# Performance work log

Measured on AMD Instinct MI355X. Metric: run time of the kernel, lower is better.

The kernel has to match this reference:

```python
import jax, jax.numpy as jnp
import numpy as np

L, B, S, M, D, H, DK, FF = 4, 2, 512, 512, 1024, 16, 64, 4096


def setup_inputs() -> dict:
    key = jax.random.key(0)
    ks = jax.random.split(key, 16)
    std = 0.02
    inp = {
        'x': jax.random.normal(ks[0], (B, S, D), jnp.float32),
        'memory': jax.random.normal(ks[1], (L, B, M, D), jnp.float32),
        'Wq': jax.random.normal(ks[2], (L, D, D), jnp.float32) * std,
        'Wk': jax.random.normal(ks[3], (L, D, D), jnp.float32) * std,
        'Wv': jax.random.normal(ks[4], (L, D, D), jnp.float32) * std,
        'Wr': jax.random.normal(ks[5], (L, D, D), jnp.float32) * std,
        'Wo': jax.random.normal(ks[6], (L, D, D), jnp.float32) * std,
        'r_w_bias': jax.random.normal(ks[7], (L, H, DK), jnp.float32) * std,
        'r_r_bias': jax.random.normal(ks[8], (L, H, DK), jnp.float32) * std,
        'ln1_g': jnp.ones((L, D), jnp.float32),
        'ln1_b': jnp.zeros((L, D), jnp.float32),
        'ln2_g': jnp.ones((L, D), jnp.float32),
        'ln2_b': jnp.zeros((L, D), jnp.float32),
        'W1': jax.random.normal(ks[9], (L, D, FF), jnp.float32) * std,
        'b1': jnp.zeros((L, FF), jnp.float32),
        'W2': jax.random.normal(ks[10], (L, FF, D), jnp.float32) * std,
        'b2': jnp.zeros((L, D), jnp.float32),
    }
    return inp


def _pos_encodings(length, hidden):
    # sinusoidal encodings over [length-1 .. 0], sin/cos concat -> [length, hidden]
    pos = jnp.arange(length - 1, -1, -1, dtype=jnp.float32)
    freqs = jnp.arange(0, hidden, 2, dtype=jnp.float32)
    inv_freq = 1.0 / (10000.0 ** (freqs / hidden))
    ang = pos[:, None] * inv_freq[None, :]  # [T, D/2]
    return jnp.concatenate([jnp.sin(ang), jnp.cos(ang)], axis=-1)  # [T, D]


def _rel_shift(x):
    # x: [B, H, T1, T2] -> Transformer-XL relative shift
    b, h, t1, t2 = x.shape
    x = jnp.pad(x, ((0, 0), (0, 0), (0, 0), (1, 0)))
    x = x.reshape(b, h, t2 + 1, t1)[:, :, 1:]
    return x.reshape(b, h, t1, t2)


def _layernorm(x, g, b, eps=1e-5):
    mu = jnp.mean(x, axis=-1, keepdims=True)
    var = jnp.var(x, axis=-1, keepdims=True)
    return (x - mu) * jax.lax.rsqrt(var + eps) * g + b


def reference(x, memory, Wq, Wk, Wv, Wr, Wo, r_w_bias, r_r_bias,
              ln1_g, ln1_b, ln2_g, ln2_b, W1, b1, W2, b2):
    T = S + M
    pos = _pos_encodings(T, D)  # [T, D]
    # future mask with zero block for memory columns: [1,1,S,T]
    fut = jnp.triu(jnp.ones((S, S), jnp.float32), k=1) * (-1e6)
    mask = jnp.concatenate([jnp.zeros((S, M), jnp.float32), fut], axis=1)[None, None]
    scale = DK ** (-0.5)

    h = x
    for l in range(L):
        kv_in = jnp.concatenate([memory[l], h], axis=1)  # [B, T, D]
        q = jnp.einsum('bsd,dhk->bhsk', h, Wq[l].reshape(D, H, DK)) * scale
        k = jnp.einsum('btd,dhk->bhtk', kv_in, Wk[l].reshape(D, H, DK))
        v = jnp.einsum('btd,dhk->bhtk', kv_in, Wv[l].reshape(D, H, DK))
        r = jnp.einsum('td,dhk->htk', pos, Wr[l].reshape(D, H, DK))

        content = jnp.einsum('bhsk,bhtk->bhst', q + r_w_bias[l][None, :, None, :], k)
        rel = jnp.einsum('bhsk,htk->bhst', q + r_r_bias[l][None, :, None, :], r)
        logits = content + _rel_shift(rel) + mask  # [B,H,S,T]
        w = jax.nn.softmax(logits, axis=-1)
        attn = jnp.einsum('bhst,bhtk->bshk', w, v).reshape(B, S, D)
        attn = attn @ Wo[l]  # merge linear
        h = _layernorm(h + attn, ln1_g[l], ln1_b[l])

        ff = jax.nn.relu(h @ W1[l] + b1[l]) @ W2[l] + b2[l]
        h = _layernorm(h + ff, ln2_g[l], ln2_b[l])
    return h
```

## Files before the change

### kernel.cpp

```cpp
#include <hip/hip_runtime.h>
#include <math.h>

#define CB  2
#define CS  512
#define CM  512
#define CD  1024
#define CH  16
#define CDK 64
#define CFF 4096
#define CL  4
#define CT  1024

using short8 = __attribute__((ext_vector_type(8))) short;
using f32x4  = __attribute__((ext_vector_type(4))) float;

__device__ __forceinline__ ushort f2bf(float x) {
    union { float f; unsigned int u; } c; c.f = x;
    unsigned int u = c.u + 0x7FFFu + ((c.u >> 16) & 1u);
    return (ushort)(u >> 16);
}
__device__ __forceinline__ float bf2f(ushort h) {
    union { unsigned int u; float f; } c; c.u = ((unsigned int)h) << 16;
    return c.f;
}

#define GLD16(gsrc, ldst) \
    __builtin_amdgcn_global_load_lds((const __attribute__((address_space(1))) void*)(gsrc), \
                                     (__attribute__((address_space(3))) void*)(ldst), 16, 0, 0)

__global__ void pos_kernel(ushort* __restrict__ pos) {
    int idx = blockIdx.x * blockDim.x + threadIdx.x;
    if (idx >= CT * (CD / 2)) return;
    int i = idx % (CD / 2);
    int t = idx / (CD / 2);
    float p = (float)(CT - 1 - t);
    float inv = __expf(-(float)i * (9.210340371976184f / 512.0f));
    float ang = p * inv;
    pos[(size_t)t * CD + i]          = f2bf(sinf(ang));
    pos[(size_t)t * CD + i + CD / 2] = f2bf(cosf(ang));
}

__global__ void concat_bf16_kernel(const float* __restrict__ mem, const float* __restrict__ h,
                                   ushort* __restrict__ kv) {
    int idx = blockIdx.x * blockDim.x + threadIdx.x;
    const int D8 = CD / 8;
    if (idx >= CB * CT * D8) return;
    int d8 = idx % D8;
    int bt = idx / D8;
    int t = bt % CT;
    int b = bt / CT;
    const float* src = (t < CM) ? &mem[((size_t)(b * CM + t)) * CD + d8 * 8]
                                : &h[((size_t)(b * CS + (t - CM))) * CD + d8 * 8];
    float4 a = *(const float4*)src;
    float4 c = *(const float4*)(src + 4);
    union { ushort us[8]; uint4 q; } pk;
    pk.us[0] = f2bf(a.x); pk.us[1] = f2bf(a.y); pk.us[2] = f2bf(a.z); pk.us[3] = f2bf(a.w);
    pk.us[4] = f2bf(c.x); pk.us[5] = f2bf(c.y); pk.us[6] = f2bf(c.z); pk.us[7] = f2bf(c.w);
    ((uint4*)kv)[idx] = pk.q;
}

__global__ __launch_bounds__(256)
void transpose_cvt(const float* __restrict__ inb, ushort* __restrict__ outb,
                   int Kd, int Nc, size_t inz, size_t outz) {
    const float* in = inb + (size_t)blockIdx.z * inz;
    ushort* o = outb + (size_t)blockIdx.z * outz;
    __shared__ __align__(16) float t[64][68];
    const int n0 = blockIdx.x * 64, k0 = blockIdx.y * 64;
    const int tid = threadIdx.x;
    #pragma unroll
    for (int rep = 0; rep < 4; ++rep) {
        int lin = rep * 256 + tid;
        int r = lin >> 4, c4 = lin & 15;
        float4 v = *(const float4*)&in[(size_t)(k0 + r) * Nc + n0 + c4 * 4];
        *(float4*)&t[r][c4 * 4] = v;
    }
    __syncthreads();
    #pragma unroll
    for (int rep = 0; rep < 2; ++rep) {
        int lin = rep * 256 + tid;
        int n = lin >> 3, kc = lin & 7;
        union { ushort us[8]; uint4 q; } pk;
        #pragma unroll
        for (int j = 0; j < 8; ++j) pk.us[j] = f2bf(t[kc * 8 + j][n]);
        *(uint4*)&o[(size_t)(n0 + n) * Kd + k0 + kc * 8] = pk.q;
    }
}

template<int BM, int BN>
__global__ __launch_bounds__(256)
void gemm_bf16(const ushort* __restrict__ A, const ushort* __restrict__ Bt,
               float* __restrict__ Cf, ushort* __restrict__ Cbf,
               int Nc, int Kd, int lda, size_t az, size_t bz, size_t cz,
               const float* __restrict__ bias, float scale, int relu)
{
    constexpr int FM = BM / 32, FN = BN / 32;
    __shared__ __align__(16) ushort As[2][BM * 64];
    __shared__ __align__(16) ushort Bs[2][BN * 64];
    const int tid  = threadIdx.x;
    const int lane = tid & 63, w = tid >> 6;
    const int wr = w >> 1, wc = w & 1;
    const int lo4 = lane & 15, g = lane >> 4;
    const int row0 = blockIdx.y * BM, col0 = blockIdx.x * BN;
    const int zz = blockIdx.z;
    const ushort* Ab = A  + (size_t)row0 * lda + (size_t)zz * az;
    const ushort* Bb = Bt + (size_t)col0 * lda + (size_t)zz * bz;
    f32x4 acc[FM][FN];
    #pragma unroll
    for (int m = 0; m < FM; ++m)
        #pragma unroll
        for (int n = 0; n < FN; ++n) acc[m][n] = (f32x4){0.f, 0.f, 0.f, 0.f};

#define GSTAGE(buf, kk) do {                                                          \
        _Pragma("unroll")                                                             \
        for (int c = 0; c < BM / 32; ++c) {                                           \
            const int linw = (c * 4 + w) * 64;                                        \
            const int lin  = linw + lane;                                             \
            GLD16(Ab + (size_t)(lin >> 3) * lda + (kk) + ((lin ^ (lin >> 3)) & 7) * 8, \
                  &As[buf][linw * 8]);                                                \
        }                                                                             \
        _Pragma("unroll")                                                             \
        for (int c = 0; c < BN / 32; ++c) {                                           \
            const int linw = (c * 4 + w) * 64;                                        \
            const int lin  = linw + lane;                                             \
            GLD16(Bb + (size_t)(lin >> 3) * lda + (kk) + ((lin ^ (lin >> 3)) & 7) * 8, \
                  &Bs[buf][linw * 8]);                                                \
        }                                                                             \
    } while (0)

    GSTAGE(0, 0);
    __syncthreads();
    int cur = 0;
    for (int k0 = 0; k0 < Kd; k0 += 64) {
        if (k0 + 64 < Kd) GSTAGE(cur ^ 1, k0 + 64);
        #pragma unroll
        for (int h2 = 0; h2 < 2; ++h2) {
            short8 af[FM], bfr[FN];
            #pragma unroll
            for (int m = 0; m < FM; ++m) {
                const int ar = wr * (BM / 2) + m * 16 + lo4;
                af[m] = *(const short8*)&As[cur][ar * 64 + ((((h2 << 2) + g) ^ (ar & 7)) << 3)];
            }
            #pragma unroll
            for (int n = 0; n < FN; ++n) {
                const int br = wc * (BN / 2) + n * 16 + lo4;
                bfr[n] = *(const short8*)&Bs[cur][br * 64 + ((((h2 << 2) + g) ^ (br & 7)) << 3)];
            }
            __builtin_amdgcn_s_setprio(1);
            #pragma unroll
            for (int m = 0; m < FM; ++m)
                #pragma unroll
                for (int n = 0; n < FN; ++n)
                    acc[m][n] = __builtin_amdgcn_mfma_f32_16x16x32_bf16(af[m], bfr[n], acc[m][n], 0, 0, 0);
            __builtin_amdgcn_s_setprio(0);
        }
        __syncthreads();
        cur ^= 1;
    }
#undef GSTAGE

    float*  Cw  = Cf  ? Cf  + (size_t)zz * cz : nullptr;
    ushort* Cbw = Cbf ? Cbf + (size_t)zz * cz : nullptr;
    const int colbase = col0 + wc * (BN / 2) + lo4;
    const int rowbase = row0 + wr * (BM / 2) + (g << 2);
    #pragma unroll
    for (int n = 0; n < FN; ++n) {
        const int col = colbase + n * 16;
        const float bv = bias ? bias[col] : 0.f;
        #pragma unroll
        for (int m = 0; m < FM; ++m) {
            #pragma unroll
            for (int r = 0; r < 4; ++r) {
                const int row = rowbase + m * 16 + r;
                float v = acc[m][n][r] * scale + bv;
                if (relu) v = fmaxf(v, 0.f);
                if (Cw)  Cw[(size_t)row * Nc + col] = v;
                if (Cbw) Cbw[(size_t)row * Nc + col] = f2bf(v);
            }
        }
    }
}

__global__ __launch_bounds__(256, 4)
void attn_kernel(const ushort* __restrict__ kvp, const ushort* __restrict__ rbm,
                 const float* __restrict__ rwb, const float* __restrict__ rrb,
                 float* __restrict__ pw)
{
    const int zt = blockIdx.x >> 1, js = blockIdx.x & 1;
    const int hh = blockIdx.y, bb = blockIdx.z;
    const int q0 = zt * 32;
    __shared__ __align__(16) ushort Ks[64][72];
    __shared__ __align__(16) ushort Vt[80][72];
    __shared__ __align__(16) ushort Rs[96][72];
    __shared__ __align__(16) ushort Pl[4][16][40];
    __shared__ float mB[2][16], lB[2][16];
    const int tid = threadIdx.x;
    const int lane = tid & 63, w = tid >> 6;
    const int iw = w & 1, jh = w >> 1;
    const int g = lane >> 4, lo4 = lane & 15;

    for (int idx = tid; idx < 16 * 36; idx += 256)
        *(uint*)&Vt[64 + idx / 36][(idx % 36) * 2] = 0x3F803F80u;

    short8 aqw[2], aqr[2];
    {
        const ushort* qrow = kvp + ((size_t)(bb * CT + CM + q0 + iw * 16 + lo4)) * 3072 + hh * CDK;
        const float* bw = rwb + hh * CDK;
        const float* br = rrb + hh * CDK;
        #pragma unroll
        for (int c = 0; c < 2; ++c) {
            const int kb = c * 32 + g * 8;
            uint4 qv = *(const uint4*)&qrow[kb];
            const ushort* qe = (const ushort*)&qv;
            #pragma unroll
            for (int e = 0; e < 8; ++e) {
                float qf = bf2f(qe[e]) * 0.125f;
                aqw[c][e] = (short)f2bf(qf + bw[kb + e]);
                aqr[c][e] = (short)f2bf(qf + br[kb + e]);
            }
        }
    }

    const int sr = tid >> 3, c8 = tid & 7;
    const int jp = tid & 31, c8v = tid >> 5;
    const ushort* kbase = kvp + ((size_t)bb * CT) * 3072 + 1024 + hh * CDK + c8 * 8;
    const ushort* vbase = kvp + ((size_t)bb * CT) * 3072 + 2048 + hh * CDK + c8v * 8;
    const ushort* rbase = rbm + hh * CDK + c8 * 8;

    float mr[4] = {-1e29f, -1e29f, -1e29f, -1e29f};
    f32x4 oacc[5];
    #pragma unroll
    for (int n = 0; n < 5; ++n) oacc[n] = (f32x4){0.f, 0.f, 0.f, 0.f};

    const int nt   = (q0 + 31 + CM) / 64 + 1;
    const int half = nt >> 1;
    const int t0 = js ? half : 0;
    const int t1 = js ? nt : half;

    for (int tt = t0; tt < t1; ++tt) {
        const int j0 = tt * 64;
        const int bnd = j0 + 480 - q0;
        __syncthreads();
        *(uint4*)&Ks[sr][c8 * 8]      = *(const uint4*)(kbase + (size_t)(j0 + sr) * 3072);
        *(uint4*)&Ks[32 + sr][c8 * 8] = *(const uint4*)(kbase + (size_t)(j0 + 32 + sr) * 3072);
        {
            uint4 v0 = *(const uint4*)(vbase + (size_t)(j0 + 2 * jp) * 3072);
            uint4 v1 = *(const uint4*)(vbase + (size_t)(j0 + 2 * jp + 1) * 3072);
            const ushort* p0 = (const ushort*)&v0;
            const ushort* p1 = (const ushort*)&v1;
            #pragma unroll
            for (int e = 0; e < 8; ++e)
                *(uint*)&Vt[c8v * 8 + e][2 * jp] = (uint)p0[e] | ((uint)p1[e] << 16);
        }
        #pragma unroll
        for (int rep = 0; rep < 3; ++rep) {
            int trel = bnd + rep * 32 + sr;
            trel = trel < 0 ? 0 : (trel > CT - 1 ? CT - 1 : trel);
            *(uint4*)&Rs[rep * 32 + sr][c8 * 8] = *(const uint4*)(rbase + (size_t)trel * CD);
        }
        __syncthreads();

        f32x4 sa[2];
        sa[0] = (f32x4){0.f, 0.f, 0.f, 0.f};
        sa[1] = (f32x4){0.f, 0.f, 0.f, 0.f};
        f32x4 ra[3];
        #pragma unroll
        for (int mm = 0; mm < 3; ++mm) ra[mm] = (f32x4){0.f, 0.f, 0.f, 0.f};
        const int wb16 = jh * 32 - iw * 16 + 16;
        __builtin_amdgcn_s_setprio(1);
        #pragma unroll
        for (int c = 0; c < 2; ++c) {
            #pragma unroll
            for (int m16 = 0; m16 < 2; ++m16) {
                short8 bk = *(const short8*)&Ks[jh * 32 + m16 * 16 + lo4][c * 32 + g * 8];
                sa[m16] = __builtin_amdgcn_mfma_f32_16x16x32_bf16(aqw[c], bk, sa[m16], 0, 0, 0);
            }
            #pragma unroll
            for (int mm = 0; mm < 3; ++mm) {
                short8 brr = *(const short8*)&Rs[wb16 + mm * 16 + lo4][c * 32 + g * 8];
                ra[mm] = __builtin_amdgcn_mfma_f32_16x16x32_bf16(aqr[c], brr, ra[mm], 0, 0, 0);
            }
        }
        __builtin_amdgcn_s_setprio(0);

        #pragma unroll
        for (int r = 0; r < 4; ++r) {
            const int il = 4 * g + r;
            const int dlo = lo4 + 15 - il;
            const int srcl = (lane & 48) | (dlo & 15);
            const int hi = dlo >> 4;
            float va = __shfl(ra[0][r], srcl);
            float vb = __shfl(ra[1][r], srcl);
            float vc = __shfl(ra[2][r], srcl);
            const float rel0 = hi ? vb : va;
            const float rel1 = hi ? vc : vb;
            const int ig = q0 + iw * 16 + il;
            const int jbase = j0 + jh * 32 + lo4;
            float s0 = (jbase      <= ig + CM) ? (sa[0][r] + rel0) : -1e30f;
            float s1 = (jbase + 16 <= ig + CM) ? (sa[1][r] + rel1) : -1e30f;
            float tm = fmaxf(s0, s1);
            #pragma unroll
            for (int off = 1; off < 16; off <<= 1) tm = fmaxf(tm, __shfl_xor(tm, off));
            const float mn = fmaxf(mr[r], tm);
            const float scl = __expf(mr[r] - mn);
            mr[r] = mn;
            Pl[w][il][lo4]      = f2bf(__expf(s0 - mn));
            Pl[w][il][16 + lo4] = f2bf(__expf(s1 - mn));
            #pragma unroll
            for (int n = 0; n < 5; ++n) oacc[n][r] *= scl;
        }

        __builtin_amdgcn_s_setprio(1);
        {
            short8 pa = *(const short8*)&Pl[w][lo4][g * 8];
            #pragma unroll
            for (int n = 0; n < 4; ++n) {
                short8 vb = *(const short8*)&Vt[n * 16 + lo4][jh * 32 + g * 8];
                oacc[n] = __builtin_amdgcn_mfma_f32_16x16x32_bf16(pa, vb, oacc[n], 0, 0, 0);
            }
            short8 vo = *(const short8*)&Vt[64 + lo4][jh * 32 + g * 8];
            oacc[4] = __builtin_amdgcn_mfma_f32_16x16x32_bf16(pa, vo, oacc[4], 0, 0, 0);
        }
        __builtin_amdgcn_s_setprio(0);
    }

    __syncthreads();
    float* oTmp = (float*)&Rs[0][0];
    if (jh == 1) {
        #pragma unroll
        for (int r = 0; r < 4; ++r) {
            const int il = 4 * g + r;
            #pragma unroll
            for (int n = 0; n < 4; ++n)
                oTmp[((iw * 16 + il) << 6) + n * 16 + lo4] = oacc[n][r];
            if (lo4 == 0) { mB[iw][il] = mr[r]; lB[iw][il] = oacc[4][r]; }
        }
    }
    __syncthreads();
    if (jh == 0) {
        float* pwp = pw + ((size_t)(((bb * CH + hh) * 16 + zt) * 2 + js)) * 2112;
        #pragma unroll
        for (int r = 0; r < 4; ++r) {
            const int il = 4 * g + r;
            const int row = iw * 16 + il;
            const float mBv = mB[iw][il], lBv = lB[iw][il];
            const float ms = fmaxf(mr[r], mBv);
            const float fA = __expf(mr[r] - ms);
            const float fB = __expf(mBv - ms);
            const float lt = oacc[4][r] * fA + lBv * fB;
            #pragma unroll
            for (int n = 0; n < 4; ++n)
                pwp[(row << 6) + n * 16 + lo4] =
                    oacc[n][r] * fA + oTmp[(row << 6) + n * 16 + lo4] * fB;
            if (lo4 == 0) { pwp[2048 + row] = ms; pwp[2048 + 32 + row] = lt; }
        }
    }
}

__global__ __launch_bounds__(256)
void attn_merge(const float* __restrict__ pw, ushort* __restrict__ outm) {
    const int zt = blockIdx.x, hh = blockIdx.y, bb = blockIdx.z;
    const int tid = threadIdx.x;
    const int row = tid >> 3, c8 = tid & 7;
    const float* pA = pw + ((size_t)(((bb * CH + hh) * 16 + zt) * 2 + 0)) * 2112;
    const float* pB = pA + 2112;
    const float mA = pA[2048 + row], lA = pA[2048 + 32 + row];
    const float mBv = pB[2048 + row], lBv = pB[2048 + 32 + row];
    const float ms = fmaxf(mA, mBv);
    const float fA = __expf(mA - ms);
    const float fB = __expf(mBv - ms);
    const float invl = 1.0f / (lA * fA + lBv * fB);
    float4 a0 = *(const float4*)&pA[(row << 6) + c8 * 8];
    float4 a1 = *(const float4*)&pA[(row << 6) + c8 * 8 + 4];
    float4 b0 = *(const float4*)&pB[(row << 6) + c8 * 8];
    float4 b1 = *(const float4*)&pB[(row << 6) + c8 * 8 + 4];
    union { ushort us[8]; uint4 q; } pk;
    pk.us[0] = f2bf((a0.x * fA + b0.x * fB) * invl);
    pk.us[1] = f2bf((a0.y * fA + b0.y * fB) * invl);
    pk.us[2] = f2bf((a0.z * fA + b0.z * fB) * invl);
    pk.us[3] = f2bf((a0.w * fA + b0.w * fB) * invl);
    pk.us[4] = f2bf((a1.x * fA + b1.x * fB) * invl);
    pk.us[5] = f2bf((a1.y * fA + b1.y * fB) * invl);
    pk.us[6] = f2bf((a1.z * fA + b1.z * fB) * invl);
    pk.us[7] = f2bf((a1.w * fA + b1.w * fB) * invl);
    *(uint4*)&outm[((size_t)(bb * CS + zt * 32 + row)) * CD + hh * CDK + c8 * 8] = pk.q;
}

__global__ __launch_bounds__(256)
void ln_kernel(const float* __restrict__ a, const float* __restrict__ p0,
               const float* __restrict__ p1, const float* __restrict__ bias,
               const float* __restrict__ g, const float* __restrict__ beta,
               float* __restrict__ out, ushort* __restrict__ outbf)
{
    const int row = blockIdx.x;
    const int tid = threadIdx.x;
    const size_t base = (size_t)row * CD;
    float4 xa = *(const float4*)&a[base + tid * 4];
    float4 x0v = *(const float4*)&p0[base + tid * 4];
    float4 x1v = *(const float4*)&p1[base + tid * 4];
    float4 bb = bias ? *(const float4*)&bias[tid * 4] : make_float4(0.f, 0.f, 0.f, 0.f);
    float x0 = xa.x + x0v.x + x1v.x + bb.x;
    float x1 = xa.y + x0v.y + x1v.y + bb.y;
    float x2 = xa.z + x0v.z + x1v.z + bb.z;
    float x3 = xa.w + x0v.w + x1v.w + bb.w;
    float sum = x0 + x1 + x2 + x3;
    float sq  = x0 * x0 + x1 * x1 + x2 * x2 + x3 * x3;
    #pragma unroll
    for (int off = 1; off < 64; off <<= 1) {
        sum += __shfl_xor(sum, off);
        sq  += __shfl_xor(sq, off);
    }
    __shared__ float ssum[4], ssq[4];
    const int wid = tid >> 6;
    if ((tid & 63) == 0) { ssum[wid] = sum; ssq[wid] = sq; }
    __syncthreads();
    sum = ssum[0] + ssum[1] + ssum[2] + ssum[3];
    sq  = ssq[0] + ssq[1] + ssq[2] + ssq[3];
    const float mean = sum * (1.0f / CD);
    const float var  = sq * (1.0f / CD) - mean * mean;
    const float rstd = rsqrtf(var + 1e-5f);
    float4 gv = *(const float4*)&g[tid * 4];
    float4 bv = *(const float4*)&beta[tid * 4];
    float4 r;
    r.x = (x0 - mean) * rstd * gv.x + bv.x;
    r.y = (x1 - mean) * rstd * gv.y + bv.y;
    r.z = (x2 - mean) * rstd * gv.z + bv.z;
    r.w = (x3 - mean) * rstd * gv.w + bv.w;
    *(float4*)&out[base + tid * 4] = r;
    if (outbf) {
        union { ushort us[4]; uint2 q; } pk;
        pk.us[0] = f2bf(r.x); pk.us[1] = f2bf(r.y); pk.us[2] = f2bf(r.z); pk.us[3] = f2bf(r.w);
        *(uint2*)&outbf[base + tid * 4] = pk.q;
    }
}

extern "C" void kernel_launch(void* const* d_in, const int* in_sizes, int n_in,
                              void* d_out, int out_size, void* d_ws, size_t ws_size,
                              hipStream_t stream) {
    const float* x    = (const float*)d_in[0];
    const float* memL = (const float*)d_in[1];
    const float* Wq   = (const float*)d_in[2];
    const float* Wk   = (const float*)d_in[3];
    const float* Wv   = (const float*)d_in[4];
    const float* Wr   = (const float*)d_in[5];
    const float* Wo   = (const float*)d_in[6];
    const float* rwb  = (const float*)d_in[7];
    const float* rrb  = (const float*)d_in[8];
    const float* ln1g = (const float*)d_in[9];
    const float* ln1b = (const float*)d_in[10];
    const float* ln2g = (const float*)d_in[11];
    const float* ln2b = (const float*)d_in[12];
    const float* W1   = (const float*)d_in[13];
    const float* b1   = (const float*)d_in[14];
    const float* W2   = (const float*)d_in[15];
    const float* b2   = (const float*)d_in[16];

    const size_t MEG = 1048576;
    float* h      = (float*)d_ws;
    float* p0     = h + MEG;
    float* p1     = p0 + MEG;
    float* pw     = p1 + MEG;
    ushort* hbf   = (ushort*)(pw + 1024 * 2112);
    ushort* kvbf  = hbf + MEG;
    ushort* kvproj= kvbf + 2 * MEG;
    ushort* attbf = kvproj + 6 * MEG;
    ushort* ff1bf = attbf + MEG;
    ushort* posbf = ff1bf + 4 * MEG;
    ushort* r_all = posbf + MEG;
    ushort* wqkvT = r_all + 4 * MEG;
    ushort* wrT   = wqkvT + 12 * MEG;
    ushort* woT   = wrT + 4 * MEG;
    ushort* w1T   = woT + 4 * MEG;
    ushort* w2T   = w1T + 16 * MEG;

    const size_t WD = (size_t)CD * CD;

    pos_kernel<<<(CT * (CD / 2)) / 256, 256, 0, stream>>>(posbf);
    transpose_cvt<<<dim3(16, 16, CL), 256, 0, stream>>>(Wq, wqkvT,          CD, CD, WD, 3 * WD);
    transpose_cvt<<<dim3(16, 16, CL), 256, 0, stream>>>(Wk, wqkvT + WD,     CD, CD, WD, 3 * WD);
    transpose_cvt<<<dim3(16, 16, CL), 256, 0, stream>>>(Wv, wqkvT + 2 * WD, CD, CD, WD, 3 * WD);
    transpose_cvt<<<dim3(16, 16, CL), 256, 0, stream>>>(Wr, wrT, CD, CD, WD, WD);
    transpose_cvt<<<dim3(16, 16, CL), 256, 0, stream>>>(Wo, woT, CD, CD, WD, WD);
    transpose_cvt<<<dim3(64, 16, CL), 256, 0, stream>>>(W1, w1T, CD, CFF, 4 * WD, 4 * WD);
    transpose_cvt<<<dim3(16, 64, CL), 256, 0, stream>>>(W2, w2T, CFF, CD, 4 * WD, 4 * WD);
    gemm_bf16<64, 64><<<dim3(16, 16, CL), 256, 0, stream>>>(
        posbf, wrT, nullptr, r_all, CD, CD, CD, 0, WD, (size_t)CT * CD, nullptr, 1.0f, 0);

    for (int l = 0; l < CL; ++l) {
        const float* hin = (l == 0) ? x : h;
        concat_bf16_kernel<<<(CB * CT * CD / 8) / 256, 256, 0, stream>>>(
            memL + (size_t)l * CB * CM * CD, hin, kvbf);

        gemm_bf16<64, 128><<<dim3(24, 32), 256, 0, stream>>>(
            kvbf, wqkvT + (size_t)l * 3 * WD, nullptr, kvproj,
            3 * CD, CD, CD, 0, 0, 0, nullptr, 1.0f, 0);

        attn_kernel<<<dim3(2 * CS / 32, CH, CB), 256, 0, stream>>>(
            kvproj, r_all + (size_t)l * CT * CD,
            rwb + (size_t)l * CH * CDK, rrb + (size_t)l * CH * CDK, pw);
        attn_merge<<<dim3(CS / 32, CH, CB), 256, 0, stream>>>(pw, attbf);

        gemm_bf16<64, 64><<<dim3(16, 16, 2), 256, 0, stream>>>(
            attbf, woT + (size_t)l * WD, p0, nullptr,
            CD, CD / 2, CD, CD / 2, CD / 2, MEG, nullptr, 1.0f, 0);
        ln_kernel<<<CB * CS, 256, 0, stream>>>(
            hin, p0, p1, nullptr, ln1g + (size_t)l * CD, ln1b + (size_t)l * CD, h, hbf);

        gemm_bf16<64, 128><<<dim3(32, 16), 256, 0, stream>>>(
            hbf, w1T + (size_t)l * 4 * WD, nullptr, ff1bf,
            CFF, CD, CD, 0, 0, 0, b1 + (size_t)l * CFF, 1.0f, 1);
        gemm_bf16<64, 64><<<dim3(16, 16, 2), 256, 0, stream>>>(
            ff1bf, w2T + (size_t)l * 4 * WD, p0, nullptr,
            CD, CFF / 2, CFF, CFF / 2, CFF / 2, MEG, nullptr, 1.0f, 0);
        ln_kernel<<<CB * CS, 256, 0, stream>>>(
            h, p0, p1, b2 + (size_t)l * CD, ln2g + (size_t)l * CD, ln2b + (size_t)l * CD,
            (l == CL - 1) ? (float*)d_out : h, (l == CL - 1) ? nullptr : hbf);
    }
}
```

Baseline: 600.0 us.

## Hoist memory bf16 conversion, fuse LN into KV buffer, swizzle GEMM/attention tiles

All layers' memory tensors are converted to bf16 once, up front, into a combined KV buffer. The second layernorm now writes its bf16 output straight into the next layer's KV slot, which removes the per-layer concat kernel. The five square weight transposes are merged into one launch. GEMM and attention workgroups get an XOR/stride block-ID swizzle for better cache locality. Attention K and R tiles now load directly to LDS via global_load_lds with an XOR-swizzled layout instead of padded register-staged copies, at the cost of a larger workspace and more complex indexing.

```diff
diff --git a/kernel.cpp b/kernel.cpp
--- a/kernel.cpp
+++ b/kernel.cpp
@@ -40,23 +40,74 @@
     pos[(size_t)t * CD + i + CD / 2] = f2bf(cosf(ang));
 }
 
-__global__ void concat_bf16_kernel(const float* __restrict__ mem, const float* __restrict__ h,
-                                   ushort* __restrict__ kv) {
+__global__ void memcvt_kernel(const float* __restrict__ memL, ushort* __restrict__ kvall) {
     int idx = blockIdx.x * blockDim.x + threadIdx.x;
     const int D8 = CD / 8;
-    if (idx >= CB * CT * D8) return;
     int d8 = idx % D8;
-    int bt = idx / D8;
-    int t = bt % CT;
-    int b = bt / CT;
-    const float* src = (t < CM) ? &mem[((size_t)(b * CM + t)) * CD + d8 * 8]
-                                : &h[((size_t)(b * CS + (t - CM))) * CD + d8 * 8];
+    int t  = (idx / D8) % CM;
+    int b  = (idx / (D8 * CM)) % CB;
+    int l  = idx / (D8 * CM * CB);
+    const float* src = memL + (((size_t)(l * CB + b)) * CM + t) * CD + d8 * 8;
     float4 a = *(const float4*)src;
     float4 c = *(const float4*)(src + 4);
     union { ushort us[8]; uint4 q; } pk;
     pk.us[0] = f2bf(a.x); pk.us[1] = f2bf(a.y); pk.us[2] = f2bf(a.z); pk.us[3] = f2bf(a.w);
     pk.us[4] = f2bf(c.x); pk.us[5] = f2bf(c.y); pk.us[6] = f2bf(c.z); pk.us[7] = f2bf(c.w);
-    ((uint4*)kv)[idx] = pk.q;
+    *(uint4*)&kvall[((size_t)l * CB * CT + (size_t)b * CT + t) * CD + d8 * 8] = pk.q;
+}
+
+__global__ void xcvt_kernel(const float* __restrict__ x, ushort* __restrict__ kv0) {
+    int idx = blockIdx.x * blockDim.x + threadIdx.x;
+    const int D8 = CD / 8;
+    int d8 = idx % D8;
+    int s  = (idx / D8) % CS;
+    int b  = idx / (D8 * CS);
+    const float* src = x + ((size_t)(b * CS + s)) * CD + d8 * 8;
+    float4 a = *(const float4*)src;
+    float4 c = *(const float4*)(src + 4);
+    union { ushort us[8]; uint4 q; } pk;
+    pk.us[0] = f2bf(a.x); pk.us[1] = f2bf(a.y); pk.us[2] = f2bf(a.z); pk.us[3] = f2bf(a.w);
+    pk.us[4] = f2bf(c.x); pk.us[5] = f2bf(c.y); pk.us[6] = f2bf(c.z); pk.us[7] = f2bf(c.w);
+    *(uint4*)&kv0[((size_t)b * CT + CM + s) * CD + d8 * 8] = pk.q;
+}
+
+__global__ __launch_bounds__(256)
+void transpose_w5(const float* __restrict__ Wq, const float* __restrict__ Wk,
+                  const float* __restrict__ Wv, const float* __restrict__ Wr,
+                  const float* __restrict__ Wo,
+                  ushort* __restrict__ wqkvT, ushort* __restrict__ wrT,
+                  ushort* __restrict__ woT) {
+    const size_t WD = (size_t)CD * CD;
+    const int wi = blockIdx.z / CL, l = blockIdx.z % CL;
+    const float* in;
+    ushort* o;
+    switch (wi) {
+        case 0: in = Wq + l * WD; o = wqkvT + (size_t)l * 3 * WD;      break;
+        case 1: in = Wk + l * WD; o = wqkvT + (size_t)l * 3 * WD + WD; break;
+        case 2: in = Wv + l * WD; o = wqkvT + (size_t)l * 3 * WD + 2 * WD; break;
+        case 3: in = Wr + l * WD; o = wrT + (size_t)l * WD; break;
+        default: in = Wo + l * WD; o = woT + (size_t)l * WD; break;
+    }
+    __shared__ __align__(16) float t[64][68];
+    const int n0 = blockIdx.x * 64, k0 = blockIdx.y * 64;
+    const int tid = threadIdx.x;
+    #pragma unroll
+    for (int rep = 0; rep < 4; ++rep) {
+        int lin = rep * 256 + tid;
+        int r = lin >> 4, c4 = lin & 15;
+        float4 v = *(const float4*)&in[(size_t)(k0 + r) * CD + n0 + c4 * 4];
+        *(float4*)&t[r][c4 * 4] = v;
+    }
+    __syncthreads();
+    #pragma unroll
+    for (int rep = 0; rep < 2; ++rep) {
+        int lin = rep * 256 + tid;
+        int n = lin >> 3, kc = lin & 7;
+        union { ushort us[8]; uint4 q; } pk;
+        #pragma unroll
+        for (int j = 0; j < 8; ++j) pk.us[j] = f2bf(t[kc * 8 + j][n]);
+        *(uint4*)&o[(size_t)(n0 + n) * CD + k0 + kc * 8] = pk.q;
+    }
 }
 
 __global__ __launch_bounds__(256)
@@ -100,7 +151,10 @@
     const int lane = tid & 63, w = tid >> 6;
     const int wr = w >> 1, wc = w & 1;
     const int lo4 = lane & 15, g = lane >> 4;
-    const int row0 = blockIdx.y * BM, col0 = blockIdx.x * BN;
+    const int nwg = gridDim.x * gridDim.y;
+    const int id  = blockIdx.y * gridDim.x + blockIdx.x;
+    const int swz = (id & 7) * (nwg >> 3) + (id >> 3);
+    const int row0 = (swz / gridDim.x) * BM, col0 = (swz % gridDim.x) * BN;
     const int zz = blockIdx.z;
     const ushort* Ab = A  + (size_t)row0 * lda + (size_t)zz * az;
     const ushort* Bb = Bt + (size_t)col0 * lda + (size_t)zz * bz;
@@ -185,12 +239,14 @@
                  const float* __restrict__ rwb, const float* __restrict__ rrb,
                  float* __restrict__ pw)
 {
-    const int zt = blockIdx.x >> 1, js = blockIdx.x & 1;
-    const int hh = blockIdx.y, bb = blockIdx.z;
+    const int id  = blockIdx.y * 32 + blockIdx.x;
+    const int swz = (id & 7) * 64 + (id >> 3);
+    const int zt = (swz & 31) >> 1, js = swz & 1;
+    const int hh = swz >> 5, bb = blockIdx.z;
     const int q0 = zt * 32;
-    __shared__ __align__(16) ushort Ks[64][72];
+    __shared__ __align__(16) ushort Ks[64 * 64];
+    __shared__ __align__(16) ushort Rs[96 * 64];
     __shared__ __align__(16) ushort Vt[80][72];
-    __shared__ __align__(16) ushort Rs[96][72];
     __shared__ __align__(16) ushort Pl[4][16][40];
     __shared__ float mB[2][16], lB[2][16];
     const int tid = threadIdx.x;
@@ -220,11 +276,10 @@
         }
     }
 
-    const int sr = tid >> 3, c8 = tid & 7;
     const int jp = tid & 31, c8v = tid >> 5;
-    const ushort* kbase = kvp + ((size_t)bb * CT) * 3072 + 1024 + hh * CDK + c8 * 8;
+    const ushort* kb2   = kvp + ((size_t)bb * CT) * 3072 + 1024 + hh * CDK;
     const ushort* vbase = kvp + ((size_t)bb * CT) * 3072 + 2048 + hh * CDK + c8v * 8;
-    const ushort* rbase = rbm + hh * CDK + c8 * 8;
+    const ushort* rb2   = rbm + hh * CDK;
 
     float mr[4] = {-1e29f, -1e29f, -1e29f, -1e29f};
     f32x4 oacc[5];
@@ -240,8 +295,24 @@
         const int j0 = tt * 64;
         const int bnd = j0 + 480 - q0;
         __syncthreads();
-        *(uint4*)&Ks[sr][c8 * 8]      = *(const uint4*)(kbase + (size_t)(j0 + sr) * 3072);
-        *(uint4*)&Ks[32 + sr][c8 * 8] = *(const uint4*)(kbase + (size_t)(j0 + 32 + sr) * 3072);
+        #pragma unroll
+        for (int c = 0; c < 2; ++c) {
+            const int linw = (c * 4 + w) * 64;
+            const int lin  = linw + lane;
+            const int row = lin >> 3, kc = lin & 7;
+            GLD16(kb2 + (size_t)(j0 + row) * 3072 + ((kc ^ (row & 7)) * 8),
+                  Ks + linw * 8);
+        }
+        #pragma unroll
+        for (int rep = 0; rep < 3; ++rep) {
+            const int linw = (rep * 4 + w) * 64;
+            const int lin  = linw + lane;
+            const int row = lin >> 3, kc = lin & 7;
+            int trel = bnd + row;
+            trel = trel < 0 ? 0 : (trel > CT - 1 ? CT - 1 : trel);
+            GLD16(rb2 + (size_t)trel * CD + ((kc ^ (row & 7)) * 8),
+                  Rs + linw * 8);
+        }
         {
             uint4 v0 = *(const uint4*)(vbase + (size_t)(j0 + 2 * jp) * 3072);
             uint4 v1 = *(const uint4*)(vbase + (size_t)(j0 + 2 * jp + 1) * 3072);
@@ -251,12 +322,6 @@
             for (int e = 0; e < 8; ++e)
                 *(uint*)&Vt[c8v * 8 + e][2 * jp] = (uint)p0[e] | ((uint)p1[e] << 16);
         }
-        #pragma unroll
-        for (int rep = 0; rep < 3; ++rep) {
-            int trel = bnd + rep * 32 + sr;
-            trel = trel < 0 ? 0 : (trel > CT - 1 ? CT - 1 : trel);
-            *(uint4*)&Rs[rep * 32 + sr][c8 * 8] = *(const uint4*)(rbase + (size_t)trel * CD);
-        }
         __syncthreads();
 
         f32x4 sa[2];
@@ -271,12 +336,14 @@
         for (int c = 0; c < 2; ++c) {
             #pragma unroll
             for (int m16 = 0; m16 < 2; ++m16) {
-                short8 bk = *(const short8*)&Ks[jh * 32 + m16 * 16 + lo4][c * 32 + g * 8];
+                const int krow = jh * 32 + m16 * 16 + lo4;
+                short8 bk = *(const short8*)&Ks[krow * 64 + ((((c << 2) + g) ^ (krow & 7)) << 3)];
                 sa[m16] = __builtin_amdgcn_mfma_f32_16x16x32_bf16(aqw[c], bk, sa[m16], 0, 0, 0);
             }
             #pragma unroll
             for (int mm = 0; mm < 3; ++mm) {
-                short8 brr = *(const short8*)&Rs[wb16 + mm * 16 + lo4][c * 32 + g * 8];
+                const int rrow = wb16 + mm * 16 + lo4;
+                short8 brr = *(const short8*)&Rs[rrow * 64 + ((((c << 2) + g) ^ (rrow & 7)) << 3)];
                 ra[mm] = __builtin_amdgcn_mfma_f32_16x16x32_bf16(aqr[c], brr, ra[mm], 0, 0, 0);
             }
         }
@@ -324,7 +391,7 @@
     }
 
     __syncthreads();
-    float* oTmp = (float*)&Rs[0][0];
+    float* oTmp = (float*)&Rs[0];
     if (jh == 1) {
         #pragma unroll
         for (int r = 0; r < 4; ++r) {
@@ -389,7 +456,8 @@
 void ln_kernel(const float* __restrict__ a, const float* __restrict__ p0,
                const float* __restrict__ p1, const float* __restrict__ bias,
                const float* __restrict__ g, const float* __restrict__ beta,
-               float* __restrict__ out, ushort* __restrict__ outbf)
+               float* __restrict__ out, ushort* __restrict__ outbf,
+               ushort* __restrict__ kvdst)
 {
     const int row = blockIdx.x;
     const int tid = threadIdx.x;
@@ -426,10 +494,12 @@
     r.z = (x2 - mean) * rstd * gv.z + bv.z;
     r.w = (x3 - mean) * rstd * gv.w + bv.w;
     *(float4*)&out[base + tid * 4] = r;
-    if (outbf) {
-        union { ushort us[4]; uint2 q; } pk;
-        pk.us[0] = f2bf(r.x); pk.us[1] = f2bf(r.y); pk.us[2] = f2bf(r.z); pk.us[3] = f2bf(r.w);
-        *(uint2*)&outbf[base + tid * 4] = pk.q;
+    union { ushort us[4]; uint2 q; } pk;
+    pk.us[0] = f2bf(r.x); pk.us[1] = f2bf(r.y); pk.us[2] = f2bf(r.z); pk.us[3] = f2bf(r.w);
+    if (outbf) *(uint2*)&outbf[base + tid * 4] = pk.q;
+    if (kvdst) {
+        const int b = row >> 9, s = row & 511;
+        *(uint2*)&kvdst[((size_t)(b * CT + CM + s)) * CD + tid * 4] = pk.q;
     }
 }
 
@@ -460,8 +530,8 @@
     float* p1     = p0 + MEG;
     float* pw     = p1 + MEG;
     ushort* hbf   = (ushort*)(pw + 1024 * 2112);
-    ushort* kvbf  = hbf + MEG;
-    ushort* kvproj= kvbf + 2 * MEG;
+    ushort* kvall = hbf + MEG;
+    ushort* kvproj= kvall + 8 * MEG;
     ushort* attbf = kvproj + 6 * MEG;
     ushort* ff1bf = attbf + MEG;
     ushort* posbf = ff1bf + 4 * MEG;
@@ -475,11 +545,9 @@
     const size_t WD = (size_t)CD * CD;
 
     pos_kernel<<<(CT * (CD / 2)) / 256, 256, 0, stream>>>(posbf);
-    transpose_cvt<<<dim3(16, 16, CL), 256, 0, stream>>>(Wq, wqkvT,          CD, CD, WD, 3 * WD);
-    transpose_cvt<<<dim3(16, 16, CL), 256, 0, stream>>>(Wk, wqkvT + WD,     CD, CD, WD, 3 * WD);
-    transpose_cvt<<<dim3(16, 16, CL), 256, 0, stream>>>(Wv, wqkvT + 2 * WD, CD, CD, WD, 3 * WD);
-    transpose_cvt<<<dim3(16, 16, CL), 256, 0, stream>>>(Wr, wrT, CD, CD, WD, WD);
-    transpose_cvt<<<dim3(16, 16, CL), 256, 0, stream>>>(Wo, woT, CD, CD, WD, WD);
+    memcvt_kernel<<<(CL * CB * CM * CD / 8) / 256, 256, 0, stream>>>(memL, kvall);
+    xcvt_kernel<<<(CB * CS * CD / 8) / 256, 256, 0, stream>>>(x, kvall);
+    transpose_w5<<<dim3(16, 16, 5 * CL), 256, 0, stream>>>(Wq, Wk, Wv, Wr, Wo, wqkvT, wrT, woT);
     transpose_cvt<<<dim3(64, 16, CL), 256, 0, stream>>>(W1, w1T, CD, CFF, 4 * WD, 4 * WD);
     transpose_cvt<<<dim3(16, 64, CL), 256, 0, stream>>>(W2, w2T, CFF, CD, 4 * WD, 4 * WD);
     gemm_bf16<64, 64><<<dim3(16, 16, CL), 256, 0, stream>>>(
@@ -487,11 +555,9 @@
 
     for (int l = 0; l < CL; ++l) {
         const float* hin = (l == 0) ? x : h;
-        concat_bf16_kernel<<<(CB * CT * CD / 8) / 256, 256, 0, stream>>>(
-            memL + (size_t)l * CB * CM * CD, hin, kvbf);
 
         gemm_bf16<64, 128><<<dim3(24, 32), 256, 0, stream>>>(
-            kvbf, wqkvT + (size_t)l * 3 * WD, nullptr, kvproj,
+            kvall + (size_t)l * 2 * MEG, wqkvT + (size_t)l * 3 * WD, nullptr, kvproj,
             3 * CD, CD, CD, 0, 0, 0, nullptr, 1.0f, 0);
 
         attn_kernel<<<dim3(2 * CS / 32, CH, CB), 256, 0, stream>>>(
@@ -503,7 +569,8 @@
             attbf, woT + (size_t)l * WD, p0, nullptr,
             CD, CD / 2, CD, CD / 2, CD / 2, MEG, nullptr, 1.0f, 0);
         ln_kernel<<<CB * CS, 256, 0, stream>>>(
-            hin, p0, p1, nullptr, ln1g + (size_t)l * CD, ln1b + (size_t)l * CD, h, hbf);
+            hin, p0, p1, nullptr, ln1g + (size_t)l * CD, ln1b + (size_t)l * CD,
+            h, hbf, nullptr);
 
         gemm_bf16<64, 128><<<dim3(32, 16), 256, 0, stream>>>(
             hbf, w1T + (size_t)l * 4 * WD, nullptr, ff1bf,
@@ -513,6 +580,7 @@
             CD, CFF / 2, CFF, CFF / 2, CFF / 2, MEG, nullptr, 1.0f, 0);
         ln_kernel<<<CB * CS, 256, 0, stream>>>(
             h, p0, p1, b2 + (size_t)l * CD, ln2g + (size_t)l * CD, ln2b + (size_t)l * CD,
-            (l == CL - 1) ? (float*)d_out : h, (l == CL - 1) ? nullptr : hbf);
-    }
-}
+            (l == CL - 1) ? (float*)d_out : h, nullptr,
+            (l == CL - 1) ? nullptr : kvall + (size_t)(l + 1) * 2 * MEG);
+    }
+}
```

After: 571.6 us. -4.7%, faster.
